# Optimization experiments

Measured on AMD Instinct MI355X. Metric: run time of the kernel, lower is better.

Reference implementation:

```python
import jax, jax.numpy as jnp
import numpy as np

B, S, HID = 2, 2048, 2048
HQ, HKV, D = 32, 4, 128
EPS = 1e-6
SCALE = D ** -0.5


def _rms_norm(x, w):
    # per-head RMSNorm over last dim, computed in fp32 like the torch module
    xf = x.astype(jnp.float32)
    var = jnp.mean(xf * xf, axis=-1, keepdims=True)
    return (w * (xf * jax.lax.rsqrt(var + EPS))).astype(x.dtype)


def _rotate_half(x):
    x1, x2 = jnp.split(x, 2, axis=-1)
    return jnp.concatenate([-x2, x1], axis=-1)


def setup_inputs() -> dict:
    key = jax.random.key(0)
    ks = jax.random.split(key, 8)
    hidden_states = jax.random.normal(ks[0], (B, S, HID), dtype=jnp.float32)
    # RoPE tables (HF Qwen style, theta=1e6)
    inv_freq = 1.0 / (1e6 ** (np.arange(0, D, 2, dtype=np.float32) / D))
    t = np.arange(S, dtype=np.float32)
    freqs = np.outer(t, inv_freq)                      # [S, D/2]
    emb = np.concatenate([freqs, freqs], axis=-1)      # [S, D]
    cos = jnp.asarray(np.cos(emb))
    sin = jnp.asarray(np.sin(emb))
    sd = HID ** -0.5
    wq = jax.random.normal(ks[1], (HID, HQ * D), dtype=jnp.float32) * sd
    wk = jax.random.normal(ks[2], (HID, HKV * D), dtype=jnp.float32) * sd
    wv = jax.random.normal(ks[3], (HID, HKV * D), dtype=jnp.float32) * sd
    wo = jax.random.normal(ks[4], (HQ * D, HID), dtype=jnp.float32) * ((HQ * D) ** -0.5)
    q_norm_w = jnp.ones((D,), dtype=jnp.float32)
    k_norm_w = jnp.ones((D,), dtype=jnp.float32)
    return {"hidden_states": hidden_states, "cos": cos, "sin": sin,
            "wq": wq, "wk": wk, "wv": wv, "wo": wo,
            "q_norm_w": q_norm_w, "k_norm_w": k_norm_w}


def reference(hidden_states, cos, sin, wq, wk, wv, wo, q_norm_w, k_norm_w):
    b, s, _ = hidden_states.shape
    # QKV projection (no bias)
    q = (hidden_states @ wq).reshape(b, s, HQ, D)
    k = (hidden_states @ wk).reshape(b, s, HKV, D)
    v = (hidden_states @ wv).reshape(b, s, HKV, D)
    # per-head RMSNorm on q, k
    q = _rms_norm(q, q_norm_w)
    k = _rms_norm(k, k_norm_w)
    # RoPE: cos/sin [s, D] -> broadcast over batch and heads
    c = cos[None, :, None, :]
    sn = sin[None, :, None, :]
    q = q * c + _rotate_half(q) * sn
    k = k * c + _rotate_half(k) * sn
    # [b, h, s, d]
    q = q.transpose(0, 2, 1, 3)
    k = k.transpose(0, 2, 1, 3)
    v = v.transpose(0, 2, 1, 3)
    # GQA: repeat kv heads to match query heads
    groups = HQ // HKV
    k = jnp.repeat(k, groups, axis=1)
    v = jnp.repeat(v, groups, axis=1)
    # causal SDPA (prefill)
    scores = jnp.einsum('bhqd,bhkd->bhqk', q, k) * SCALE
    causal = jnp.tril(jnp.ones((s, s), dtype=bool))
    scores = jnp.where(causal[None, None], scores, jnp.finfo(scores.dtype).min)
    attn = jax.nn.softmax(scores, axis=-1)
    out = jnp.einsum('bhqk,bhkd->bhqd', attn, v)
    out = out.transpose(0, 2, 1, 3).reshape(b, s, HQ * D)
    return out @ wo
```

## Files before the change

### kernel.cpp

```cpp
#include <hip/hip_runtime.h>
#include <hip/hip_bf16.h>
#include <stdint.h>

typedef __bf16 bf16;
typedef __bf16 bf16x4 __attribute__((ext_vector_type(4)));
typedef __bf16 bf16x8 __attribute__((ext_vector_type(8)));
typedef float floatx4 __attribute__((ext_vector_type(4)));

#define MFMA16(a, b, c) __builtin_amdgcn_mfma_f32_16x16x32_bf16((a), (b), (c), 0, 0, 0)

static __device__ __forceinline__ void async_load16(const bf16* g, bf16* l) {
    __builtin_amdgcn_global_load_lds(
        (const __attribute__((address_space(1))) uint32_t*)(const void*)g,
        (__attribute__((address_space(3))) uint32_t*)(void*)l,
        16, 0, 0);
}

static __device__ __forceinline__ bf16x8 load8(const bf16* p) {
    return *(const bf16x8*)p;
}
static __device__ __forceinline__ bf16x8 load8(const float* p) {
    const float4 a = *(const float4*)p;
    const float4 b = *(const float4*)(p + 4);
    bf16x8 r;
    r[0] = (bf16)a.x; r[1] = (bf16)a.y; r[2] = (bf16)a.z; r[3] = (bf16)a.w;
    r[4] = (bf16)b.x; r[5] = (bf16)b.y; r[6] = (bf16)b.z; r[7] = (bf16)b.w;
    return r;
}

__global__ __launch_bounds__(256) void f2b(const float* __restrict__ in,
                                           bf16* __restrict__ out) {
    const size_t i = ((size_t)blockIdx.x * 256 + threadIdx.x) * 8;
    *(bf16x8*)&out[i] = load8(in + i);
}

__global__ __launch_bounds__(256) void transposeF2B(const float* __restrict__ in,
                                                    bf16* __restrict__ out,
                                                    int R, int C) {
    __shared__ float t[32][33];
    const int c0 = blockIdx.x * 32, r0 = blockIdx.y * 32;
    const int tx = threadIdx.x & 31, ty = threadIdx.x >> 5;
#pragma unroll
    for (int i = 0; i < 4; i++)
        t[ty + i * 8][tx] = in[(size_t)(r0 + ty + i * 8) * C + c0 + tx];
    __syncthreads();
#pragma unroll
    for (int i = 0; i < 4; i++)
        out[(size_t)(c0 + ty + i * 8) * R + r0 + tx] = (bf16)t[tx][ty + i * 8];
}

__global__ __launch_bounds__(256) void gemm_qkv(const bf16* __restrict__ A,
                                                const bf16* __restrict__ BT,
                                                bf16* __restrict__ Q,
                                                bf16* __restrict__ K2,
                                                bf16* __restrict__ Vt) {
    constexpr int K = 2048;
    __shared__ __attribute__((aligned(16))) bf16 As[128 * 64];
    __shared__ __attribute__((aligned(16))) bf16 Bs[128 * 64];
    const int tid = threadIdx.x;
    const int wave = tid >> 6, lane = tid & 63;
    const int quad = lane >> 4, l16 = lane & 15;
    const int m0 = blockIdx.y * 128, n0 = blockIdx.x * 128;
    const int wr = (wave >> 1) * 64, wc = (wave & 1) * 64;

    floatx4 acc[4][4] = {};

    const int wbase = wave * 32;
    const bf16* aSrc[4]; const bf16* bSrc[4];
#pragma unroll
    for (int j = 0; j < 4; j++) {
        const int r = wbase + 8 * j + (lane >> 3);
        aSrc[j] = A + (size_t)(m0 + r) * K + (((lane & 7) ^ (r & 7)) << 3);
        bSrc[j] = BT + (size_t)(n0 + r) * K + (((lane & 7) ^ (r & 7)) << 3);
    }
    bf16* aDst = &As[wbase * 64];
    bf16* bDst = &Bs[wbase * 64];

    for (int k0 = 0; k0 < K; k0 += 64) {
#pragma unroll
        for (int j = 0; j < 4; j++) {
            async_load16(aSrc[j] + k0, aDst + j * 8 * 64);
            async_load16(bSrc[j] + k0, bDst + j * 8 * 64);
        }
        __syncthreads();

#pragma unroll
        for (int ks = 0; ks < 2; ks++) {
            const int slot = ((ks * 4 + quad) ^ (l16 & 7)) << 3;
            bf16x8 af[4], bfr[4];
#pragma unroll
            for (int i = 0; i < 4; i++)
                af[i] = *(const bf16x8*)&As[(wr + i * 16 + l16) * 64 + slot];
#pragma unroll
            for (int j = 0; j < 4; j++)
                bfr[j] = *(const bf16x8*)&Bs[(wc + j * 16 + l16) * 64 + slot];
#pragma unroll
            for (int i = 0; i < 4; i++)
#pragma unroll
                for (int j = 0; j < 4; j++)
                    acc[i][j] = MFMA16(af[i], bfr[j], acc[i][j]);
        }
        __syncthreads();
    }

    const int region = (n0 >= 4608) ? 2 : (n0 >= 4096 ? 1 : 0);
#pragma unroll
    for (int i = 0; i < 4; i++) {
#pragma unroll
        for (int j = 0; j < 4; j++) {
            const int row = m0 + wr + i * 16 + quad * 4;
            const int col = n0 + wc + j * 16 + l16;
            if (region == 0) {
#pragma unroll
                for (int r = 0; r < 4; r++)
                    Q[(size_t)(row + r) * 4096 + col] = (bf16)acc[i][j][r];
            } else if (region == 1) {
#pragma unroll
                for (int r = 0; r < 4; r++)
                    K2[(size_t)(row + r) * 512 + (col - 4096)] = (bf16)acc[i][j][r];
            } else {
                bf16x4 t;
#pragma unroll
                for (int r = 0; r < 4; r++) t[r] = (bf16)acc[i][j][r];
                *(bf16x4*)&Vt[(size_t)(col - 4608) * 4096 + row] = t;
            }
        }
    }
}

__global__ __launch_bounds__(256) void gemm_o(const bf16* __restrict__ A,
                                              const bf16* __restrict__ BT,
                                              float* __restrict__ C) {
    constexpr int K = 4096, N = 2048;
    __shared__ __attribute__((aligned(16))) bf16 As[128 * 64];
    __shared__ __attribute__((aligned(16))) bf16 Bs[128 * 64];
    const int tid = threadIdx.x;
    const int wave = tid >> 6, lane = tid & 63;
    const int quad = lane >> 4, l16 = lane & 15;
    const int m0 = blockIdx.y * 128, n0 = blockIdx.x * 128;
    const int wr = (wave >> 1) * 64, wc = (wave & 1) * 64;

    floatx4 acc[4][4] = {};

    const int wbase = wave * 32;
    const bf16* aSrc[4]; const bf16* bSrc[4];
#pragma unroll
    for (int j = 0; j < 4; j++) {
        const int r = wbase + 8 * j + (lane >> 3);
        aSrc[j] = A + (size_t)(m0 + r) * K + (((lane & 7) ^ (r & 7)) << 3);
        bSrc[j] = BT + (size_t)(n0 + r) * K + (((lane & 7) ^ (r & 7)) << 3);
    }
    bf16* aDst = &As[wbase * 64];
    bf16* bDst = &Bs[wbase * 64];

    for (int k0 = 0; k0 < K; k0 += 64) {
#pragma unroll
        for (int j = 0; j < 4; j++) {
            async_load16(aSrc[j] + k0, aDst + j * 8 * 64);
            async_load16(bSrc[j] + k0, bDst + j * 8 * 64);
        }
        __syncthreads();

#pragma unroll
        for (int ks = 0; ks < 2; ks++) {
            const int slot = ((ks * 4 + quad) ^ (l16 & 7)) << 3;
            bf16x8 af[4], bfr[4];
#pragma unroll
            for (int i = 0; i < 4; i++)
                af[i] = *(const bf16x8*)&As[(wr + i * 16 + l16) * 64 + slot];
#pragma unroll
            for (int j = 0; j < 4; j++)
                bfr[j] = *(const bf16x8*)&Bs[(wc + j * 16 + l16) * 64 + slot];
#pragma unroll
            for (int i = 0; i < 4; i++)
#pragma unroll
                for (int j = 0; j < 4; j++)
                    acc[i][j] = MFMA16(af[i], bfr[j], acc[i][j]);
        }
        __syncthreads();
    }

#pragma unroll
    for (int i = 0; i < 4; i++) {
#pragma unroll
        for (int j = 0; j < 4; j++) {
            const int row = m0 + wr + i * 16 + quad * 4;
            const int col = n0 + wc + j * 16 + l16;
#pragma unroll
            for (int r = 0; r < 4; r++)
                C[(size_t)(row + r) * N + col] = acc[i][j][r];
        }
    }
}

__global__ __launch_bounds__(256) void rmsrope(bf16* __restrict__ x,
                                               const float* __restrict__ w,
                                               const float* __restrict__ cosb,
                                               const float* __restrict__ sinb,
                                               int nh, int S) {
    const int lane = threadIdx.x & 63;
    const int row = blockIdx.x * 4 + (threadIdx.x >> 6);
    const int s = (row / nh) % S;
    bf16* p = x + (size_t)row * 128;
    float x1 = (float)p[lane];
    float x2 = (float)p[lane + 64];
    float ssq = x1 * x1 + x2 * x2;
#pragma unroll
    for (int m = 1; m < 64; m <<= 1) ssq += __shfl_xor(ssq, m);
    const float r = rsqrtf(ssq * (1.0f / 128.0f) + 1e-6f);
    const float y1 = w[lane] * x1 * r;
    const float y2 = w[lane + 64] * x2 * r;
    const float c1 = cosb[s * 128 + lane];
    const float s1 = sinb[s * 128 + lane];
    const float c2 = cosb[s * 128 + lane + 64];
    const float s2 = sinb[s * 128 + lane + 64];
    p[lane] = (bf16)(y1 * c1 - y2 * s1);
    p[lane + 64] = (bf16)(y2 * c2 + y1 * s2);
}

__global__ __launch_bounds__(512, 4) void attn(bf16* QO,
                                               const bf16* __restrict__ Km,
                                               const bf16* __restrict__ Vt,
                                               int S) {
    __shared__ __attribute__((aligned(16))) bf16 Kl[2][64 * 128];
    __shared__ __attribute__((aligned(16))) bf16 Vl[2][128 * 64];
    __shared__ __attribute__((aligned(16))) bf16 Pl[8][16 * 40];

    const int tid = threadIdx.x, wave = tid >> 6, lane = tid & 63;
    const int quad = lane >> 4, l16 = lane & 15;
    const int h = blockIdx.y, b = blockIdx.z;
    const int kvh = h >> 3;
    const float scale = 0.08838834764831845f;

    const bf16* Kg = Km + (size_t)b * S * 512 + kvh * 128;
    const bf16* Vg = Vt + (size_t)kvh * 128 * 4096 + (size_t)b * S;

    const int krow0 = wave * 8 + (lane >> 4);
    const int krow1 = wave * 8 + 4 + (lane >> 4);
    const bf16* kSrc0 = Kg + (size_t)krow0 * 512 + (((lane & 15) ^ (krow0 & 7)) << 3);
    const bf16* kSrc1 = Kg + (size_t)krow1 * 512 + (((lane & 15) ^ (krow1 & 7)) << 3);
    const int vrow0 = wave * 16 + (lane >> 3);
    const int vrow1 = wave * 16 + 8 + (lane >> 3);
    const bf16* vSrc0 = Vg + (size_t)vrow0 * 4096 + (((lane & 7) ^ (vrow0 & 7)) << 3);
    const bf16* vSrc1 = Vg + (size_t)vrow1 * 4096 + (((lane & 7) ^ (vrow1 & 7)) << 3);

#define STAGE(buf, kk)                                                  \
    do {                                                                \
        bf16* kb_ = &Kl[buf][(wave * 8) * 128];                         \
        bf16* vb_ = &Vl[buf][(wave * 16) * 64];                         \
        async_load16(kSrc0 + (size_t)(kk) * 512, kb_);                  \
        async_load16(kSrc1 + (size_t)(kk) * 512, kb_ + 4 * 128);        \
        async_load16(vSrc0 + (kk), vb_);                                \
        async_load16(vSrc1 + (kk), vb_ + 8 * 64);                       \
    } while (0)

    bf16* pw = &Pl[wave][0];

#pragma unroll
    for (int half = 0; half < 2; half++) {
        const int qt = half ? (15 - blockIdx.x) : blockIdx.x;
        const int qb = qt * 128 + wave * 16;

        bf16x8 qf[4];
        {
            const bf16* qrow = QO + (size_t)(b * S + qb + l16) * 4096 + h * 128 + quad * 8;
#pragma unroll
            for (int c = 0; c < 4; c++) qf[c] = *(const bf16x8*)(qrow + c * 32);
        }

        floatx4 o_acc[8] = {};
        float l_i[4] = {0.f, 0.f, 0.f, 0.f};

        const int nt = 2 * (qt + 1);
        STAGE(0, 0);

        for (int kt = 0; kt < nt; ++kt) {
            const int k0 = kt * 64;
            const int cur = kt & 1;
            if (kt + 1 < nt) {
                STAGE(cur ^ 1, (kt + 1) * 64);
                asm volatile("s_waitcnt vmcnt(4)" ::: "memory");
            } else {
                asm volatile("s_waitcnt vmcnt(0)" ::: "memory");
            }
            __builtin_amdgcn_s_barrier();
            __builtin_amdgcn_sched_barrier(0);

            if (k0 <= qb + 15) {
                const bf16* kl = &Kl[cur][0];
                const bf16* vl = &Vl[cur][0];

                floatx4 sc[4] = {};
#pragma unroll
                for (int c = 0; c < 4; c++) {
                    const int slot = ((c * 4 + quad) ^ (l16 & 7)) << 3;
#pragma unroll
                    for (int m = 0; m < 4; m++) {
                        const bf16x8 kf = *(const bf16x8*)&kl[(l16 + 16 * m) * 128 + slot];
                        sc[m] = MFMA16(qf[c], kf, sc[m]);
                    }
                }

#pragma unroll
                for (int ks = 0; ks < 2; ks++) {
                    const int kb = k0 + ks * 32;
                    if (kb > qb + 15) continue;
                    const floatx4 s0 = sc[2 * ks], s1 = sc[2 * ks + 1];
                    if (kb + 31 > qb) {
#pragma unroll
                        for (int r = 0; r < 4; r++) {
                            const int qi = qb + quad * 4 + r;
                            const float p0 = (kb + l16 > qi) ? 0.f : __expf(s0[r] * scale);
                            const float p1 = (kb + 16 + l16 > qi) ? 0.f : __expf(s1[r] * scale);
                            l_i[r] += p0 + p1;
                            pw[(quad * 4 + r) * 40 + l16] = (bf16)p0;
                            pw[(quad * 4 + r) * 40 + l16 + 16] = (bf16)p1;
                        }
                    } else {
#pragma unroll
                        for (int r = 0; r < 4; r++) {
                            const float p0 = __expf(s0[r] * scale);
                            const float p1 = __expf(s1[r] * scale);
                            l_i[r] += p0 + p1;
                            pw[(quad * 4 + r) * 40 + l16] = (bf16)p0;
                            pw[(quad * 4 + r) * 40 + l16 + 16] = (bf16)p1;
                        }
                    }
                    const bf16x8 pa = *(const bf16x8*)&pw[l16 * 40 + quad * 8];
#pragma unroll
                    for (int c = 0; c < 8; c++) {
                        const int vps = ((ks * 4 + quad) ^ (l16 & 7)) << 3;
                        const bf16x8 vf = *(const bf16x8*)&vl[(c * 16 + l16) * 64 + vps];
                        o_acc[c] = MFMA16(pa, vf, o_acc[c]);
                    }
                }
            }
            __builtin_amdgcn_s_barrier();
        }

#pragma unroll
        for (int r = 0; r < 4; r++) {
            float l = l_i[r];
            l += __shfl_xor(l, 1);
            l += __shfl_xor(l, 2);
            l += __shfl_xor(l, 4);
            l += __shfl_xor(l, 8);
            const float inv = (l > 0.f) ? 1.0f / l : 0.f;
            const size_t orow = (size_t)(b * S + qb + quad * 4 + r) * 4096 + h * 128;
#pragma unroll
            for (int c = 0; c < 8; c++)
                QO[orow + c * 16 + l16] = (bf16)(o_acc[c][r] * inv);
        }
    }
#undef STAGE
}

template <typename TA, typename TB, typename TC>
__global__ __launch_bounds__(256) void gemm_bn(const TA* __restrict__ A,
                                               const TB* __restrict__ B,
                                               TC* __restrict__ C,
                                               int M, int N, int K) {
    __shared__ __attribute__((aligned(16))) bf16 As[128 * 32];
    __shared__ __attribute__((aligned(16))) bf16 Bs[128 * 32];
    const int tid = threadIdx.x;
    const int wave = tid >> 6, lane = tid & 63;
    const int quad = lane >> 4, l16 = lane & 15;
    const int m0 = blockIdx.y * 128, n0 = blockIdx.x * 128;
    const int wr = (wave >> 1) * 64, wc = (wave & 1) * 64;
    floatx4 acc[4][4] = {};
    const int r0 = tid >> 2;
    const int kc = (tid & 3) * 8;
    const TA* gA0 = A + (size_t)(m0 + r0) * K + kc;
    const TA* gA1 = A + (size_t)(m0 + 64 + r0) * K + kc;
    const int kr = tid & 31;
    const int nc8 = (tid >> 5) * 8;
    const TB* gB = B + (size_t)kr * N + n0 + nc8;
    for (int k0 = 0; k0 < K; k0 += 32) {
        const bf16x8 a0 = load8(gA0 + k0);
        const bf16x8 a1 = load8(gA1 + k0);
        const TB* gBk = gB + (size_t)k0 * N;
        const bf16x8 b0 = load8(gBk);
        const bf16x8 b1 = load8(gBk + 64);
        __syncthreads();
        *(bf16x8*)&As[r0 * 32 + kc] = a0;
        *(bf16x8*)&As[(64 + r0) * 32 + kc] = a1;
#pragma unroll
        for (int j = 0; j < 8; j++) {
            Bs[(nc8 + j) * 32 + kr] = b0[j];
            Bs[(nc8 + 64 + j) * 32 + kr] = b1[j];
        }
        __syncthreads();
        bf16x8 af[4], bfr[4];
#pragma unroll
        for (int i = 0; i < 4; i++)
            af[i] = *(const bf16x8*)&As[(wr + i * 16 + l16) * 32 + quad * 8];
#pragma unroll
        for (int j = 0; j < 4; j++)
            bfr[j] = *(const bf16x8*)&Bs[(wc + j * 16 + l16) * 32 + quad * 8];
#pragma unroll
        for (int i = 0; i < 4; i++)
#pragma unroll
            for (int j = 0; j < 4; j++)
                acc[i][j] = MFMA16(af[i], bfr[j], acc[i][j]);
    }
#pragma unroll
    for (int i = 0; i < 4; i++) {
#pragma unroll
        for (int j = 0; j < 4; j++) {
            const int row = m0 + wr + i * 16 + quad * 4;
            const int col = n0 + wc + j * 16 + l16;
#pragma unroll
            for (int r = 0; r < 4; r++)
                C[(size_t)(row + r) * N + col] = (TC)acc[i][j][r];
        }
    }
}

__global__ __launch_bounds__(256) void attn_fb(bf16* QO,
                                               const bf16* __restrict__ Km,
                                               const bf16* __restrict__ Vm,
                                               int S) {
    __shared__ __attribute__((aligned(16))) bf16 Kl[32 * 136];
    __shared__ __attribute__((aligned(16))) bf16 Vl[128 * 40];
    __shared__ __attribute__((aligned(16))) bf16 Pl[4][16 * 40];
    const int tid = threadIdx.x, wave = tid >> 6, lane = tid & 63;
    const int quad = lane >> 4, l16 = lane & 15;
    const int q0 = blockIdx.x * 64;
    const int h = blockIdx.y, b = blockIdx.z;
    const int kvh = h >> 3;
    const int q_base = q0 + wave * 16;
    const float scale = 0.08838834764831845f;
    bf16x8 qf[4];
    {
        const bf16* qrow = QO + (size_t)(b * S + q_base + l16) * 4096 + h * 128 + quad * 8;
#pragma unroll
        for (int c = 0; c < 4; c++) qf[c] = *(const bf16x8*)(qrow + c * 32);
    }
    floatx4 o_acc[8] = {};
    float l_i[4] = {0.f, 0.f, 0.f, 0.f};
    const int kend = q0 + 64;
    for (int k0 = 0; k0 < kend; k0 += 32) {
#pragma unroll
        for (int it = 0; it < 2; ++it) {
            const int cc = tid + it * 256;
            const int row = cc >> 4;
            const int off = (cc & 15) * 8;
            const size_t gidx = (size_t)(b * S + k0 + row) * 512 + kvh * 128 + off;
            const bf16x8 kv = *(const bf16x8*)&Km[gidx];
            const bf16x8 vv = *(const bf16x8*)&Vm[gidx];
            *(bf16x8*)&Kl[row * 136 + off] = kv;
#pragma unroll
            for (int j = 0; j < 8; j++) Vl[(off + j) * 40 + row] = vv[j];
        }
        __syncthreads();
        if (k0 <= q_base + 15) {
            floatx4 sc0 = {}, sc1 = {};
#pragma unroll
            for (int c = 0; c < 4; c++) {
                bf16x8 b0 = *(const bf16x8*)&Kl[l16 * 136 + c * 32 + quad * 8];
                bf16x8 b1 = *(const bf16x8*)&Kl[(l16 + 16) * 136 + c * 32 + quad * 8];
                sc0 = MFMA16(qf[c], b0, sc0);
                sc1 = MFMA16(qf[c], b1, sc1);
            }
            const bool edge = (k0 + 31 > q_base);
            bf16* pw = &Pl[wave][0];
#pragma unroll
            for (int r = 0; r < 4; r++) {
                const int qi = q_base + quad * 4 + r;
                const bool mk0 = edge && (k0 + l16 > qi);
                const bool mk1 = edge && (k0 + 16 + l16 > qi);
                const float p0 = mk0 ? 0.f : __expf(sc0[r] * scale);
                const float p1 = mk1 ? 0.f : __expf(sc1[r] * scale);
                l_i[r] += p0 + p1;
                pw[(quad * 4 + r) * 40 + l16] = (bf16)p0;
                pw[(quad * 4 + r) * 40 + l16 + 16] = (bf16)p1;
            }
            const bf16x8 pa = *(const bf16x8*)&pw[l16 * 40 + quad * 8];
#pragma unroll
            for (int c = 0; c < 8; c++) {
                const bf16x8 vf = *(const bf16x8*)&Vl[(c * 16 + l16) * 40 + quad * 8];
                o_acc[c] = MFMA16(pa, vf, o_acc[c]);
            }
        }
        __syncthreads();
    }
#pragma unroll
    for (int r = 0; r < 4; r++) {
        float l = l_i[r];
        l += __shfl_xor(l, 1);
        l += __shfl_xor(l, 2);
        l += __shfl_xor(l, 4);
        l += __shfl_xor(l, 8);
        const float inv = (l > 0.f) ? 1.0f / l : 0.f;
        const size_t orow = (size_t)(b * S + q_base + quad * 4 + r) * 4096 + h * 128;
#pragma unroll
        for (int c = 0; c < 8; c++)
            QO[orow + c * 16 + l16] = (bf16)(o_acc[c][r] * inv);
    }
}

extern "C" void kernel_launch(void* const* d_in, const int* in_sizes, int n_in,
                              void* d_out, int out_size, void* d_ws, size_t ws_size,
                              hipStream_t stream) {
    const float* hidden = (const float*)d_in[0];
    const float* cosb = (const float*)d_in[1];
    const float* sinb = (const float*)d_in[2];
    const float* wq = (const float*)d_in[3];
    const float* wk = (const float*)d_in[4];
    const float* wv = (const float*)d_in[5];
    const float* wo = (const float*)d_in[6];
    const float* qnw = (const float*)d_in[7];
    const float* knw = (const float*)d_in[8];
    float* out = (float*)d_out;

    constexpr int B = 2, S = 2048, HID = 2048, HQ = 32, HKV = 4, D = 128;
    constexpr int M = B * S;
    constexpr int NQ = HQ * D;
    constexpr int NKV = HKV * D;
    constexpr int NQKV = NQ + 2 * NKV;

    const size_t need = ((size_t)NQKV * HID + (size_t)HID * NQ +
                         (size_t)M * NQ + 2 * (size_t)M * NKV) * sizeof(bf16);

    if (ws_size >= need) {
        bf16* p = (bf16*)d_ws;
        bf16* wqkvT = p; p += (size_t)NQKV * HID;
        bf16* X = p;     p += (size_t)HID * NQ;
        bf16* Qb = p;    p += (size_t)M * NQ;
        bf16* Kb = p;    p += (size_t)M * NKV;
        bf16* Vt = p;    p += (size_t)NKV * M;

        transposeF2B<<<dim3(NQ / 32, HID / 32), 256, 0, stream>>>(wq, wqkvT, HID, NQ);
        transposeF2B<<<dim3(NKV / 32, HID / 32), 256, 0, stream>>>(wk, wqkvT + (size_t)NQ * HID, HID, NKV);
        transposeF2B<<<dim3(NKV / 32, HID / 32), 256, 0, stream>>>(wv, wqkvT + (size_t)(NQ + NKV) * HID, HID, NKV);

        f2b<<<dim3((M * HID) / (256 * 8)), 256, 0, stream>>>(hidden, X);

        gemm_qkv<<<dim3(NQKV / 128, M / 128), 256, 0, stream>>>(X, wqkvT, Qb, Kb, Vt);

        rmsrope<<<dim3(M * HQ / 4), 256, 0, stream>>>(Qb, qnw, cosb, sinb, HQ, S);
        rmsrope<<<dim3(M * HKV / 4), 256, 0, stream>>>(Kb, knw, cosb, sinb, HKV, S);

        attn<<<dim3(S / 256, HQ, B), 512, 0, stream>>>(Qb, Kb, Vt, S);

        transposeF2B<<<dim3(HID / 32, NQ / 32), 256, 0, stream>>>(wo, X, NQ, HID);
        gemm_o<<<dim3(HID / 128, M / 128), 256, 0, stream>>>(Qb, X, out);
    } else {
        bf16* p = (bf16*)d_ws;
        bf16* Qb = p;  p += (size_t)M * NQ;
        bf16* Kb = p;  p += (size_t)M * NKV;
        bf16* Vb = p;  p += (size_t)M * NKV;

        gemm_bn<float, float, bf16><<<dim3(NQ / 128, M / 128), 256, 0, stream>>>(hidden, wq, Qb, M, NQ, HID);
        gemm_bn<float, float, bf16><<<dim3(NKV / 128, M / 128), 256, 0, stream>>>(hidden, wk, Kb, M, NKV, HID);
        gemm_bn<float, float, bf16><<<dim3(NKV / 128, M / 128), 256, 0, stream>>>(hidden, wv, Vb, M, NKV, HID);
        rmsrope<<<dim3(M * HQ / 4), 256, 0, stream>>>(Qb, qnw, cosb, sinb, HQ, S);
        rmsrope<<<dim3(M * HKV / 4), 256, 0, stream>>>(Kb, knw, cosb, sinb, HKV, S);
        attn_fb<<<dim3(S / 64, HQ, B), 256, 0, stream>>>(Qb, Kb, Vb, S);
        gemm_bn<bf16, float, float><<<dim3(HID / 128, M / 128), 256, 0, stream>>>(Qb, wo, out, M, HID, NQ);
    }
}
```

Before: 465.0 us.

## Double-buffer LDS tiles in QKV and output-projection GEMMs

```diff
diff --git a/kernel.cpp b/kernel.cpp
--- a/kernel.cpp
+++ b/kernel.cpp
@@ -55,8 +55,8 @@
                                                 bf16* __restrict__ K2,
                                                 bf16* __restrict__ Vt) {
     constexpr int K = 2048;
-    __shared__ __attribute__((aligned(16))) bf16 As[128 * 64];
-    __shared__ __attribute__((aligned(16))) bf16 Bs[128 * 64];
+    __shared__ __attribute__((aligned(16))) bf16 As[2][128 * 64];
+    __shared__ __attribute__((aligned(16))) bf16 Bs[2][128 * 64];
     const int tid = threadIdx.x;
     const int wave = tid >> 6, lane = tid & 63;
     const int quad = lane >> 4, l16 = lane & 15;
@@ -73,16 +73,30 @@
         aSrc[j] = A + (size_t)(m0 + r) * K + (((lane & 7) ^ (r & 7)) << 3);
         bSrc[j] = BT + (size_t)(n0 + r) * K + (((lane & 7) ^ (r & 7)) << 3);
     }
-    bf16* aDst = &As[wbase * 64];
-    bf16* bDst = &Bs[wbase * 64];
-
-    for (int k0 = 0; k0 < K; k0 += 64) {
-#pragma unroll
-        for (int j = 0; j < 4; j++) {
-            async_load16(aSrc[j] + k0, aDst + j * 8 * 64);
-            async_load16(bSrc[j] + k0, bDst + j * 8 * 64);
-        }
-        __syncthreads();
+
+#define GSTAGE(buf, kk)                                                 \
+    do {                                                                \
+        bf16* aD_ = &As[buf][wbase * 64];                               \
+        bf16* bD_ = &Bs[buf][wbase * 64];                               \
+        _Pragma("unroll")                                               \
+        for (int j_ = 0; j_ < 4; j_++) {                                \
+            async_load16(aSrc[j_] + (kk), aD_ + j_ * 8 * 64);           \
+            async_load16(bSrc[j_] + (kk), bD_ + j_ * 8 * 64);           \
+        }                                                               \
+    } while (0)
+
+    constexpr int NKT = K / 64;
+    GSTAGE(0, 0);
+    int cur = 0;
+    for (int kt = 0; kt < NKT; ++kt) {
+        if (kt + 1 < NKT) {
+            GSTAGE(cur ^ 1, (kt + 1) * 64);
+            asm volatile("s_waitcnt vmcnt(8)" ::: "memory");
+        } else {
+            asm volatile("s_waitcnt vmcnt(0)" ::: "memory");
+        }
+        __builtin_amdgcn_s_barrier();
+        __builtin_amdgcn_sched_barrier(0);
 
 #pragma unroll
         for (int ks = 0; ks < 2; ks++) {
@@ -90,18 +104,20 @@
             bf16x8 af[4], bfr[4];
 #pragma unroll
             for (int i = 0; i < 4; i++)
-                af[i] = *(const bf16x8*)&As[(wr + i * 16 + l16) * 64 + slot];
+                af[i] = *(const bf16x8*)&As[cur][(wr + i * 16 + l16) * 64 + slot];
 #pragma unroll
             for (int j = 0; j < 4; j++)
-                bfr[j] = *(const bf16x8*)&Bs[(wc + j * 16 + l16) * 64 + slot];
+                bfr[j] = *(const bf16x8*)&Bs[cur][(wc + j * 16 + l16) * 64 + slot];
 #pragma unroll
             for (int i = 0; i < 4; i++)
 #pragma unroll
                 for (int j = 0; j < 4; j++)
                     acc[i][j] = MFMA16(af[i], bfr[j], acc[i][j]);
         }
-        __syncthreads();
-    }
+        __builtin_amdgcn_s_barrier();
+        cur ^= 1;
+    }
+#undef GSTAGE
 
     const int region = (n0 >= 4608) ? 2 : (n0 >= 4096 ? 1 : 0);
 #pragma unroll
@@ -132,8 +148,8 @@
                                               const bf16* __restrict__ BT,
                                               float* __restrict__ C) {
     constexpr int K = 4096, N = 2048;
-    __shared__ __attribute__((aligned(16))) bf16 As[128 * 64];
-    __shared__ __attribute__((aligned(16))) bf16 Bs[128 * 64];
+    __shared__ __attribute__((aligned(16))) bf16 As[2][128 * 64];
+    __shared__ __attribute__((aligned(16))) bf16 Bs[2][128 * 64];
     const int tid = threadIdx.x;
     const int wave = tid >> 6, lane = tid & 63;
     const int quad = lane >> 4, l16 = lane & 15;
@@ -150,16 +166,30 @@
         aSrc[j] = A + (size_t)(m0 + r) * K + (((lane & 7) ^ (r & 7)) << 3);
         bSrc[j] = BT + (size_t)(n0 + r) * K + (((lane & 7) ^ (r & 7)) << 3);
     }
-    bf16* aDst = &As[wbase * 64];
-    bf16* bDst = &Bs[wbase * 64];
-
-    for (int k0 = 0; k0 < K; k0 += 64) {
-#pragma unroll
-        for (int j = 0; j < 4; j++) {
-            async_load16(aSrc[j] + k0, aDst + j * 8 * 64);
-            async_load16(bSrc[j] + k0, bDst + j * 8 * 64);
-        }
-        __syncthreads();
+
+#define GSTAGE(buf, kk)                                                 \
+    do {                                                                \
+        bf16* aD_ = &As[buf][wbase * 64];                               \
+        bf16* bD_ = &Bs[buf][wbase * 64];                               \
+        _Pragma("unroll")                                               \
+        for (int j_ = 0; j_ < 4; j_++) {                                \
+            async_load16(aSrc[j_] + (kk), aD_ + j_ * 8 * 64);           \
+            async_load16(bSrc[j_] + (kk), bD_ + j_ * 8 * 64);           \
+        }                                                               \
+    } while (0)
+
+    constexpr int NKT = K / 64;
+    GSTAGE(0, 0);
+    int cur = 0;
+    for (int kt = 0; kt < NKT; ++kt) {
+        if (kt + 1 < NKT) {
+            GSTAGE(cur ^ 1, (kt + 1) * 64);
+            asm volatile("s_waitcnt vmcnt(8)" ::: "memory");
+        } else {
+            asm volatile("s_waitcnt vmcnt(0)" ::: "memory");
+        }
+        __builtin_amdgcn_s_barrier();
+        __builtin_amdgcn_sched_barrier(0);
 
 #pragma unroll
         for (int ks = 0; ks < 2; ks++) {
@@ -167,18 +197,20 @@
             bf16x8 af[4], bfr[4];
 #pragma unroll
             for (int i = 0; i < 4; i++)
-                af[i] = *(const bf16x8*)&As[(wr + i * 16 + l16) * 64 + slot];
+                af[i] = *(const bf16x8*)&As[cur][(wr + i * 16 + l16) * 64 + slot];
 #pragma unroll
             for (int j = 0; j < 4; j++)
-                bfr[j] = *(const bf16x8*)&Bs[(wc + j * 16 + l16) * 64 + slot];
+                bfr[j] = *(const bf16x8*)&Bs[cur][(wc + j * 16 + l16) * 64 + slot];
 #pragma unroll
             for (int i = 0; i < 4; i++)
 #pragma unroll
                 for (int j = 0; j < 4; j++)
                     acc[i][j] = MFMA16(af[i], bfr[j], acc[i][j]);
         }
-        __syncthreads();
-    }
+        __builtin_amdgcn_s_barrier();
+        cur ^= 1;
+    }
+#undef GSTAGE
 
 #pragma unroll
     for (int i = 0; i < 4; i++) {
```

After: 474.4 us. +2.0%, slower.
